# Kernel optimization log

Hardware: AMD Instinct MI355X
Metric: run time of the kernel (lower is better)

## Reference

```python
import jax, jax.numpy as jnp
import numpy as np
import math

D_MODEL = 256; N_LEVELS = 5; N_HEADS = 8; N_POINTS = 4
D_HEAD = D_MODEL // N_HEADS
BS = 1; T = 5; H = 64; W = 96


def conv3x3(x, w, b):
    # x: (N, C, H, W), w: (O, C, 3, 3) -> SAME padding conv
    y = jax.lax.conv_general_dilated(x, w, (1, 1), ((1, 1), (1, 1)),
                                     dimension_numbers=('NCHW', 'OIHW', 'NCHW'))
    return y + b[None, :, None, None]


def bilinear_zero(img, px, py):
    # img: (C, Hh, Ww); px, py: (...) pixel coords; zero padding outside.
    C, Hh, Ww = img.shape
    x0 = jnp.floor(px); y0 = jnp.floor(py)
    wx1 = px - x0; wx0 = 1.0 - wx1
    wy1 = py - y0; wy0 = 1.0 - wy1

    def gather(xi, yi):
        valid = (xi >= 0) & (xi < Ww) & (yi >= 0) & (yi < Hh)
        xc = jnp.clip(xi, 0, Ww - 1).astype(jnp.int32)
        yc = jnp.clip(yi, 0, Hh - 1).astype(jnp.int32)
        return img[:, yc, xc] * valid.astype(img.dtype)

    return (gather(x0, y0) * (wx0 * wy0) + gather(x0 + 1, y0) * (wx1 * wy0)
            + gather(x0, y0 + 1) * (wx0 * wy1) + gather(x0 + 1, y0 + 1) * (wx1 * wy1))


def warp(x, flo):
    # x: (b, c, h, w), flo: (b, 2, h, w); grid_sample(align_corners=True) equivalent
    b, c, h, w = x.shape
    gy, gx = jnp.meshgrid(jnp.arange(h, dtype=x.dtype), jnp.arange(w, dtype=x.dtype), indexing='ij')
    px = gx[None] + flo[:, 0]
    py = gy[None] + flo[:, 1]
    return jax.vmap(bilinear_zero)(x, px, py)


def flow_guid_offset(ff, fb, offset):
    # ff, fb: (b, 4, 2, h, w); offset: (N, T*h*w, heads, L, P, 2)
    N, THW, heads, L, P, _ = offset.shape
    hw = THW // L
    off = offset.reshape(N, L, hw, heads, L, P, 2)
    f01, f12, f23, f34 = ff[:, 0], ff[:, 1], ff[:, 2], ff[:, 3]
    f02 = f01 + warp(f12, f01)
    f03 = f02 + warp(f23, f02)
    f04 = f03 + warp(f34, f03)
    f13 = f12 + warp(f23, f12)
    f14 = f13 + warp(f34, f13)
    f24 = f23 + warp(f34, f23)
    b10, b21, b32, b43 = fb[:, 0], fb[:, 1], fb[:, 2], fb[:, 3]
    b42 = b43 + warp(b32, b43)
    b41 = b42 + warp(b21, b42)
    b40 = b41 + warp(b10, b41)
    b31 = b32 + warp(b21, b32)
    b30 = b31 + warp(b10, b31)
    b20 = b21 + warp(b10, b21)

    def flat(f):  # (b, 2, h, w) -> (b, hw, 2)
        return f.transpose(0, 2, 3, 1).reshape(f.shape[0], -1, 2)

    z = jnp.zeros_like(flat(f01))
    adds = jnp.stack([
        jnp.stack([z, flat(f01), flat(f02), flat(f03), flat(f04)], axis=2),
        jnp.stack([flat(b10), z, flat(f12), flat(f13), flat(f14)], axis=2),
        jnp.stack([flat(b20), flat(b21), z, flat(f23), flat(f24)], axis=2),
        jnp.stack([flat(b30), flat(b31), flat(b32), z, flat(f34)], axis=2),
        # NOTE: source repeats chunk3's flows for chunk4 (kept faithfully)
        jnp.stack([flat(b30), flat(b31), flat(b32), z, flat(f34)], axis=2),
    ], axis=1)  # (b, L, hw, L, 2)
    off = off + adds[:, :, :, None, :, None, :]
    return off.reshape(N, THW, heads, L, P, 2)


def _forward(query, input_flatten, reference_points, input_spatial_shapes,
             input_level_start_index, input_padding_mask, flow_forward, flow_backward,
             w_off, b_off, w_attn, b_attn, w_val, b_val, w_out, b_out):
    bs, t, c, h, w = query.shape
    q2 = query.reshape(bs * t, c, h, w)
    value = conv3x3(input_flatten.reshape(bs * t, c, h, w), w_val, b_val)
    off = conv3x3(q2, w_off, b_off)      # (bs*t, heads*L*P*2, h, w)
    aw = conv3x3(q2, w_attn, b_attn)     # (bs*t, heads*L*P, h, w)
    Lq = t * h * w

    def to_tokens(x):  # (bs*t, C, h, w) -> (bs, t*h*w, C)
        return x.reshape(bs, t, -1, h * w).transpose(0, 1, 3, 2).reshape(bs, Lq, -1)

    value = to_tokens(value)
    off = to_tokens(off)
    aw = to_tokens(aw)
    value = jnp.where(input_padding_mask[..., None], jnp.zeros((), value.dtype), value)
    value = value.reshape(bs, Lq, N_HEADS, D_HEAD)
    off = off.reshape(bs, Lq, N_HEADS, N_LEVELS, N_POINTS, 2)
    off = flow_guid_offset(flow_forward, flow_backward, off)
    aw = jax.nn.softmax(aw.reshape(bs, Lq, N_HEADS, N_LEVELS * N_POINTS), axis=-1)
    aw = aw.reshape(bs, Lq, N_HEADS, N_LEVELS, N_POINTS)
    # sampling locations, normalized by (W_l, H_l)
    normalizer = jnp.stack([input_spatial_shapes[:, 1], input_spatial_shapes[:, 0]], -1).astype(off.dtype)
    loc = reference_points[:, :, None, :, None, :] + off / normalizer[None, None, None, :, None, :]
    # core: multi-scale deformable bilinear sampling (grid_sample align_corners=False)
    value_lvl = value.reshape(bs, t, h * w, N_HEADS, D_HEAD)
    out = jnp.zeros((bs * N_HEADS, D_HEAD, Lq), dtype=value.dtype)
    for lvl in range(N_LEVELS):
        v = value_lvl[:, lvl].reshape(bs, h, w, N_HEADS, D_HEAD)
        v = v.transpose(0, 3, 4, 1, 2).reshape(bs * N_HEADS, D_HEAD, h, w)
        l = loc[:, :, :, lvl]  # (bs, Lq, heads, P, 2)
        px = (l[..., 0] * w - 0.5).transpose(0, 2, 1, 3).reshape(bs * N_HEADS, Lq, N_POINTS)
        py = (l[..., 1] * h - 0.5).transpose(0, 2, 1, 3).reshape(bs * N_HEADS, Lq, N_POINTS)
        samp = jax.vmap(bilinear_zero)(v, px, py)  # (bs*heads, D_HEAD, Lq, P)
        w_l = aw[:, :, :, lvl].transpose(0, 2, 1, 3).reshape(bs * N_HEADS, 1, Lq, N_POINTS)
        out = out + jnp.sum(samp * w_l, axis=-1)
    out = out.reshape(bs, N_HEADS, D_HEAD, Lq).transpose(0, 3, 1, 2).reshape(bs, Lq, c)
    out = out.reshape(bs, t, h * w, c).transpose(0, 1, 3, 2).reshape(bs * t, c, h, w)
    out = conv3x3(out, w_out, b_out)
    return out.reshape(bs, t, c, h, w)


def setup_inputs() -> dict:
    key = jax.random.key(0)
    ks = jax.random.split(key, 10)
    Lq = T * H * W
    query = jax.random.normal(ks[0], (BS, T, D_MODEL, H, W), jnp.float32)
    input_flatten = jax.random.normal(ks[1], (BS, T, D_MODEL, H, W), jnp.float32)
    reference_points = jax.random.uniform(ks[2], (BS, Lq, N_LEVELS, 2), jnp.float32)
    input_spatial_shapes = jnp.tile(jnp.array([[H, W]], jnp.int32), (N_LEVELS, 1))
    input_level_start_index = jnp.arange(N_LEVELS, dtype=jnp.int32) * (H * W)
    input_padding_mask = jnp.zeros((BS, Lq), dtype=bool)
    flow_forward = jax.random.normal(ks[3], (BS, 4, 2, H, W), jnp.float32) * 2.0
    flow_backward = jax.random.normal(ks[4], (BS, 4, 2, H, W), jnp.float32) * 2.0

    def xavier(k, shape):
        fan_in = shape[1] * shape[2] * shape[3]
        fan_out = shape[0] * shape[2] * shape[3]
        lim = math.sqrt(6.0 / (fan_in + fan_out))
        return jax.random.uniform(k, shape, jnp.float32, -lim, lim)

    w_off = jax.random.normal(ks[5], (N_HEADS * N_LEVELS * N_POINTS * 2, D_MODEL, 3, 3), jnp.float32) * 0.01
    # bias init follows _reset_parameters grid_init
    thetas = np.arange(N_HEADS) * (2.0 * np.pi / N_HEADS)
    grid = np.stack([np.cos(thetas), np.sin(thetas)], -1)
    grid = grid / np.abs(grid).max(-1, keepdims=True)
    grid = np.tile(grid.reshape(N_HEADS, 1, 1, 2), (1, N_LEVELS, N_POINTS, 1))
    for i in range(N_POINTS):
        grid[:, :, i, :] *= i + 1
    b_off = jnp.asarray(grid.reshape(-1), jnp.float32)
    w_attn = jax.random.normal(ks[6], (N_HEADS * N_LEVELS * N_POINTS, D_MODEL, 3, 3), jnp.float32) * 0.01
    b_attn = jnp.zeros((N_HEADS * N_LEVELS * N_POINTS,), jnp.float32)
    w_val = xavier(ks[7], (D_MODEL, D_MODEL, 3, 3)); b_val = jnp.zeros((D_MODEL,), jnp.float32)
    w_out = xavier(ks[8], (D_MODEL, D_MODEL, 3, 3)); b_out = jnp.zeros((D_MODEL,), jnp.float32)
    return {"query": query, "input_flatten": input_flatten, "reference_points": reference_points,
            "input_spatial_shapes": input_spatial_shapes, "input_level_start_index": input_level_start_index,
            "input_padding_mask": input_padding_mask, "flow_forward": flow_forward, "flow_backward": flow_backward,
            "w_off": w_off, "b_off": b_off, "w_attn": w_attn, "b_attn": b_attn,
            "w_val": w_val, "b_val": b_val, "w_out": w_out, "b_out": b_out}


def reference(query, input_flatten, reference_points, input_spatial_shapes,
              input_level_start_index, input_padding_mask, flow_forward, flow_backward,
              w_off, b_off, w_attn, b_attn, w_val, b_val, w_out, b_out):
    return _forward(query, input_flatten, reference_points, input_spatial_shapes,
                    input_level_start_index, input_padding_mask, flow_forward, flow_backward,
                    w_off, b_off, w_attn, b_attn, w_val, b_val, w_out, b_out)
```

## Files before the change

### kernel.cpp

```cpp
#include <hip/hip_runtime.h>
#include <hip/hip_bf16.h>
#include <hip/hip_fp16.h>

typedef __hip_bfloat16 bf16;
typedef __attribute__((ext_vector_type(8))) short short8;
typedef __attribute__((ext_vector_type(4))) float float4v;

#define T_  5
#define H_  64
#define W_  96
#define HW_ (H_*W_)
#define C_  256
#define NH_ 8
#define DH_ 32
#define NL_ 5
#define NP_ 4
#define LQ_ (T_*HW_)
#define UNITS_ (LQ_*NH_)

#define PH_ 66
#define PW_ 98

static __device__ __forceinline__ void gl2lds16(const bf16* g, bf16* l){
  __builtin_amdgcn_global_load_lds(
      (const __attribute__((address_space(1))) unsigned int*)g,
      (__attribute__((address_space(3))) unsigned int*)l, 16, 0, 0);
}

__global__ __launch_bounds__(256) void zfill_k(float4* __restrict__ p, int n4){
  int i = blockIdx.x*256 + threadIdx.x;
  if (i < n4){ float4 z; z.x=z.y=z.z=z.w=0.f; p[i]=z; }
}

__global__ __launch_bounds__(256) void pad_in_k(const float* __restrict__ in0,
                                                const float* __restrict__ in1,
                                                bf16* __restrict__ pad0,
                                                bf16* __restrict__ pad1){
  __shared__ bf16 sb[256][66];
  const float* in = blockIdx.z ? in1 : in0;
  bf16* pad       = blockIdx.z ? pad1 : pad0;
  int t = blockIdx.y;
  int pix0 = blockIdx.x*64;
  int tid = threadIdx.x;
  int pl = tid & 63, cg = tid >> 6;
  #pragma unroll 4
  for (int it=0; it<64; ++it){
    int c = it*4 + cg;
    sb[c][pl] = __float2bfloat16(in[((size_t)t*C_ + c)*HW_ + pix0 + pl]);
  }
  __syncthreads();
  for (int p=0; p<64; ++p){
    int pix = pix0 + p;
    int y = pix/W_, x = pix - y*W_;
    pad[(((size_t)t*PH_ + y+1)*PW_ + x+1)*C_ + tid] = sb[tid][p];
  }
}

#define S0_ 589824
#define S1_ 1179648
__global__ __launch_bounds__(256) void wt_all_k(const float* __restrict__ wv,
                                                const float* __restrict__ wo,
                                                const float* __restrict__ wa,
                                                const float* __restrict__ wout,
                                                const float* __restrict__ bo,
                                                const float* __restrict__ ba,
                                                bf16* __restrict__ WTv,
                                                bf16* __restrict__ WToa,
                                                bf16* __restrict__ WTout,
                                                float* __restrict__ boa){
  int idx = blockIdx.x*256 + threadIdx.x;
  if (idx < S0_){
    int n = idx/2304, r = idx - n*2304; int tap = r>>8, ci = r&255;
    WTv[idx] = __float2bfloat16(wv[((size_t)(n*C_+ci))*9 + tap]);
  } else if (idx < S0_+S1_){
    int k = idx - S0_;
    int n = k/2304, r = k - n*2304; int tap=r>>8, ci=r&255;
    float v = 0.f;
    if (n < 320)      v = wo[((size_t)(n*C_+ci))*9+tap];
    else if (n < 480) v = wa[((size_t)((n-320)*C_+ci))*9+tap];
    WToa[k] = __float2bfloat16(v);
  } else if (idx < S0_+S1_+S0_){
    int k = idx - S0_ - S1_;
    int n = k/2304, r = k - n*2304; int tap=r>>8, ci=r&255;
    WTout[k] = __float2bfloat16(wout[((size_t)(n*C_+ci))*9+tap]);
  } else if (idx < S0_+S1_+S0_+512){
    int n = idx - (S0_+S1_+S0_);
    float v = 0.f;
    if (n < 320) v = bo[n]; else if (n < 480) v = ba[n-320];
    boa[n] = v;
  }
}

#define BM 128
#define BN 256
#define BK 64

__global__ __launch_bounds__(256,2) void gemm12_k(const bf16* __restrict__ Av,
                                                  const bf16* __restrict__ Aq,
                                                  const bf16* __restrict__ WTv,
                                                  const bf16* __restrict__ WToa,
                                                  const float* __restrict__ bv,
                                                  const float* __restrict__ boa,
                                                  bf16* __restrict__ outv,
                                                  float* __restrict__ P,
                                                  float* __restrict__ aw){
  __shared__ __align__(16) bf16 As[BM*BK];
  __shared__ __align__(16) bf16 Bs[BN*BK];
  int tid = threadIdx.x;
  int lane = tid & 63, wvi = tid >> 6;
  int wm = wvi & 1, wn = wvi >> 1;
  int quad = lane >> 4, l15 = lane & 15;
  int bx = blockIdx.x, byy = blockIdx.y;
  bool isval = byy == 0;
  const bf16* Apad  = isval ? Av  : Aq;
  const bf16* WT    = isval ? WTv : WToa;
  const float* bias = isval ? bv  : boa;
  int nby = isval ? 0 : byy - 1;

  int srow = tid >> 3;
  int c8   = (tid & 7) ^ (srow & 7);
  long abase[4];
  #pragma unroll
  for (int j=0;j<4;++j){
    int p = j*32 + srow;
    int Pm = bx*BM + p;
    int t = Pm / HW_, rem = Pm - t*HW_;
    int y = rem / W_, x = rem - y*W_;
    abase[j] = ((long)(t*PH_ + y)*PW_ + x)*C_ + c8*8;
  }
  const bf16* bbase = WT + (size_t)(nby*BN + srow)*2304 + c8*8;

  float4v acc[4][8];
  #pragma unroll
  for (int jn=0;jn<8;++jn){
    float bvv = bias[nby*BN + wn*128 + jn*16 + l15];
    #pragma unroll
    for (int i=0;i<4;++i){ acc[i][jn][0]=bvv; acc[i][jn][1]=bvv; acc[i][jn][2]=bvv; acc[i][jn][3]=bvv; }
  }

  for (int kt=0; kt<36; ++kt){
    int tap = kt >> 2, kc = (kt & 3) << 6;
    int dy = tap/3, dx = tap - dy*3;
    long ash = (long)(dy*PW_ + dx)*C_ + kc;
    long bsh = (long)kt*64;
    __syncthreads();
    #pragma unroll
    for (int j=0;j<4;++j)
      gl2lds16(Apad + abase[j] + ash, As + (j*256+tid)*8);
    #pragma unroll
    for (int j=0;j<8;++j)
      gl2lds16(bbase + (size_t)j*32*2304 + bsh, Bs + (j*256+tid)*8);
    __syncthreads();
    #pragma unroll
    for (int kk=0; kk<2; ++kk){
      int slot = ((kk<<2) + quad) ^ (l15 & 7);
      short8 af[4], bfr[8];
      #pragma unroll
      for (int jn=0;jn<8;++jn)
        bfr[jn] = *(const short8*)(Bs + (wn*128 + jn*16 + l15)*BK + slot*8);
      #pragma unroll
      for (int i=0;i<4;++i)
        af[i] = *(const short8*)(As + (wm*64 + i*16 + l15)*BK + slot*8);
      #pragma unroll
      for (int i=0;i<4;++i)
        #pragma unroll
        for (int jn=0;jn<8;++jn)
          acc[i][jn] = __builtin_amdgcn_mfma_f32_16x16x32_bf16(af[i], bfr[jn], acc[i][jn], 0,0,0);
    }
  }

  #pragma unroll
  for (int i=0;i<4;++i){
    int mr = bx*BM + wm*64 + i*16 + quad*4;
    #pragma unroll
    for (int jn=0;jn<8;++jn){
      int nc = nby*BN + wn*128 + jn*16 + l15;
      #pragma unroll
      for (int r=0;r<4;++r){
        float v = acc[i][jn][r];
        long m = mr + r;
        if (isval){
          outv[m*256 + nc] = __float2bfloat16(v);
        } else {
          if (nc < 320){
            int h = nc/40, rr = nc - h*40;
            int l = rr >> 3, pxy = rr & 7;
            P[((size_t)l*UNITS_ + m*8 + h)*8 + pxy] = v;
          } else if (nc < 480){
            int hh = (nc-320)/20, ii = (nc-320) - hh*20;
            aw[((size_t)m*8 + hh)*20 + ii] = v;
          }
        }
      }
    }
  }
}

__global__ __launch_bounds__(256,2) void gemm_out_k(const bf16* __restrict__ Apad,
                                                    const bf16* __restrict__ WT,
                                                    const float* __restrict__ bias,
                                                    float* __restrict__ out){
  __shared__ __align__(16) bf16 As[BM*BK];
  __shared__ __align__(16) bf16 Bs[BN*BK];
  int tid = threadIdx.x;
  int lane = tid & 63, wvi = tid >> 6;
  int wm = wvi & 1, wn = wvi >> 1;
  int quad = lane >> 4, l15 = lane & 15;
  int bx = blockIdx.x;

  int srow = tid >> 3;
  int c8   = (tid & 7) ^ (srow & 7);
  long abase[4];
  #pragma unroll
  for (int j=0;j<4;++j){
    int p = j*32 + srow;
    int Pm = bx*BM + p;
    int t = Pm / HW_, rem = Pm - t*HW_;
    int y = rem / W_, x = rem - y*W_;
    abase[j] = ((long)(t*PH_ + y)*PW_ + x)*C_ + c8*8;
  }
  const bf16* bbase = WT + (size_t)srow*2304 + c8*8;

  float4v acc[4][8];
  #pragma unroll
  for (int jn=0;jn<8;++jn){
    float bvv = bias[wn*128 + jn*16 + l15];
    #pragma unroll
    for (int i=0;i<4;++i){ acc[i][jn][0]=bvv; acc[i][jn][1]=bvv; acc[i][jn][2]=bvv; acc[i][jn][3]=bvv; }
  }

  for (int kt=0; kt<36; ++kt){
    int tap = kt >> 2, kc = (kt & 3) << 6;
    int dy = tap/3, dx = tap - dy*3;
    long ash = (long)(dy*PW_ + dx)*C_ + kc;
    long bsh = (long)kt*64;
    __syncthreads();
    #pragma unroll
    for (int j=0;j<4;++j)
      gl2lds16(Apad + abase[j] + ash, As + (j*256+tid)*8);
    #pragma unroll
    for (int j=0;j<8;++j)
      gl2lds16(bbase + (size_t)j*32*2304 + bsh, Bs + (j*256+tid)*8);
    __syncthreads();
    #pragma unroll
    for (int kk=0; kk<2; ++kk){
      int slot = ((kk<<2) + quad) ^ (l15 & 7);
      short8 af[4], bfr[8];
      #pragma unroll
      for (int jn=0;jn<8;++jn)
        bfr[jn] = *(const short8*)(Bs + (wn*128 + jn*16 + l15)*BK + slot*8);
      #pragma unroll
      for (int i=0;i<4;++i)
        af[i] = *(const short8*)(As + (wm*64 + i*16 + l15)*BK + slot*8);
      #pragma unroll
      for (int i=0;i<4;++i)
        #pragma unroll
        for (int jn=0;jn<8;++jn)
          acc[i][jn] = __builtin_amdgcn_mfma_f32_16x16x32_bf16(af[i], bfr[jn], acc[i][jn], 0,0,0);
    }
  }

  int t = (bx*BM) / HW_;
  #pragma unroll
  for (int i=0;i<4;++i){
    int m = bx*BM + wm*64 + i*16 + quad*4;
    int pix = m - t*HW_;
    #pragma unroll
    for (int jn=0;jn<8;++jn){
      int nc = wn*128 + jn*16 + l15;
      *(float4v*)(out + ((size_t)(t*C_ + nc))*HW_ + pix) = acc[i][jn];
    }
  }
}

static __device__ __forceinline__ float bilin2(const float* __restrict__ img,
                                               float px, float py){
  float x0f = floorf(px), y0f = floorf(py);
  int x0 = (int)x0f, y0 = (int)y0f;
  float fx = px - x0f, fy = py - y0f;
  int x1 = x0+1, y1 = y0+1;
  bool vx0 = (x0>=0)&&(x0<W_), vx1 = (x1>=0)&&(x1<W_);
  bool vy0 = (y0>=0)&&(y0<H_), vy1 = (y1>=0)&&(y1<H_);
  float c00 = (vx0&&vy0)? img[y0*W_+x0] : 0.f;
  float c10 = (vx1&&vy0)? img[y0*W_+x1] : 0.f;
  float c01 = (vx0&&vy1)? img[y1*W_+x0] : 0.f;
  float c11 = (vx1&&vy1)? img[y1*W_+x1] : 0.f;
  return c00*(1.f-fx)*(1.f-fy) + c10*fx*(1.f-fy) + c01*(1.f-fx)*fy + c11*fx*fy;
}

__global__ __launch_bounds__(256) void flow_init_k(const float* __restrict__ ff,
                                                   const float* __restrict__ fb,
                                                   float* __restrict__ flows){
  int i = blockIdx.x*256 + threadIdx.x;
  const int per = 2*HW_;
  if (i >= 7*per) return;
  int f = i/per, r = i - f*per;
  float v; int slot;
  if (f < 4) { v = ff[f*per + r]; slot = f; }
  else       { v = fb[(f-4)*per + r]; slot = 10+(f-4); }
  flows[slot*per + r] = v;
}

struct Comps { int dst[5]; int a[5]; int src[5]; };

__global__ __launch_bounds__(256) void flow_compose_k(float* __restrict__ flows, Comps c){
  int ci  = blockIdx.y;
  int pix = blockIdx.x*256 + threadIdx.x;
  float* D       = flows + c.dst[ci]*2*HW_;
  const float* A = flows + c.a[ci]  *2*HW_;
  const float* S = flows + c.src[ci]*2*HW_;
  float ax = A[pix], ay = A[HW_+pix];
  float px = (float)(pix % W_) + ax;
  float py = (float)(pix / W_) + ay;
  D[pix]      = ax + bilin2(S,      px, py);
  D[HW_+pix]  = ay + bilin2(S+HW_,  px, py);
}

__device__ const int g_slotTab[25] = {
  -1,  0,  4,  5,  6,
  10, -1,  1,  7,  8,
  13, 11, -1,  2,  9,
  15, 14, 12, -1,  3,
  15, 14, 12, -1,  3 };

__global__ __launch_bounds__(256) void prep_k(const float* __restrict__ aw,
                                              const float* __restrict__ ref,
                                              const float* __restrict__ flows,
                                              float* __restrict__ P,
                                              __half* __restrict__ w16){
  int unit = blockIdx.x*256 + threadIdx.x;
  const float4* p4 = (const float4*)(aw + (size_t)unit*20);
  float4 v[5];
  #pragma unroll
  for (int i=0;i<5;++i) v[i] = p4[i];
  float* e = (float*)v;
  float m = -1e30f;
  #pragma unroll
  for (int i=0;i<20;++i) m = fmaxf(m, e[i]);
  float s = 0.f;
  #pragma unroll
  for (int i=0;i<20;++i){ e[i] = __expf(e[i]-m); s += e[i]; }
  float inv = 1.f/s;
  __half2* o2 = (__half2*)(w16 + (size_t)unit*20);
  #pragma unroll
  for (int i=0;i<10;++i)
    o2[i] = __floats2half2_rn(e[2*i]*inv, e[2*i+1]*inv);

  int q = unit >> 3;
  int t_q = q / HW_, pix = q - t_q*HW_;
  #pragma unroll
  for (int l=0; l<NL_; ++l){
    int slot = g_slotTab[t_q*5+l];
    float ax=0.f, ay=0.f;
    if (slot >= 0){ ax = flows[slot*2*HW_ + pix]; ay = flows[slot*2*HW_ + HW_ + pix]; }
    float bx = ref[(q*5+l)*2+0]*(float)W_ - 0.5f + ax;
    float by = ref[(q*5+l)*2+1]*(float)H_ - 0.5f + ay;
    float2* pp = (float2*)(P + ((size_t)l*UNITS_ + unit)*8);
    #pragma unroll
    for (int p=0;p<4;++p){ float2 t = pp[p]; t.x += bx; t.y += by; pp[p] = t; }
  }
}

template<bool FIRST, bool LAST>
__global__ __launch_bounds__(256) void phase_k(const unsigned* __restrict__ vimg0,
                                               const float2*  __restrict__ Pl,
                                               const __half*  __restrict__ wl,
                                               __half2* __restrict__ acc,
                                               bf16* __restrict__ attn_pad){
  __shared__ float4 sW[16][4];
  __shared__ int4   sI[16][4];
  int tid = threadIdx.x;
  if (tid < 64){
    int g = tid >> 2, p = tid & 3;
    int unit = blockIdx.x*16 + g;
    float2 pp = Pl[(size_t)unit*4 + p];
    float w = __half2float(wl[(size_t)unit*20 + p]);
    float x0f = floorf(pp.x), y0f = floorf(pp.y);
    float fx = pp.x - x0f,    fy = pp.y - y0f;
    int x0 = (int)x0f, y0 = (int)y0f;
    int x1 = x0+1, y1 = y0+1;
    float wx0 = 1.f-fx, wx1 = fx, wy0 = 1.f-fy, wy1 = fy;
    if ((unsigned)x0 >= (unsigned)W_) wx0 = 0.f;
    if ((unsigned)x1 >= (unsigned)W_) wx1 = 0.f;
    if ((unsigned)y0 >= (unsigned)H_) wy0 = 0.f;
    if ((unsigned)y1 >= (unsigned)H_) wy1 = 0.f;
    int xc0 = min(max(x0,0),W_-1), xc1 = min(max(x1,0),W_-1);
    int yc0 = min(max(y0,0),H_-1), yc1 = min(max(y1,0),H_-1);
    sW[g][p] = make_float4(w*wx0*wy0, w*wx1*wy0, w*wx0*wy1, w*wx1*wy1);
    sI[g][p] = make_int4((yc0*W_+xc0)*128, (yc0*W_+xc1)*128,
                         (yc1*W_+xc0)*128, (yc1*W_+xc1)*128);
  }
  __syncthreads();
  int g = tid >> 4, e = tid & 15;
  int unit = blockIdx.x*16 + g;
  int q = unit >> 3, h = unit & 7;
  const unsigned* vimg = vimg0 + h*16 + e;
  float a0, a1;
  if (FIRST){ a0 = 0.f; a1 = 0.f; }
  else { __half2 c = acc[(size_t)unit*16 + e]; a0 = __low2float(c); a1 = __high2float(c); }
  #pragma unroll
  for (int p=0; p<4; ++p){
    float4 w4 = sW[g][p];
    int4   i4 = sI[g][p];
    unsigned u00 = vimg[i4.x], u10 = vimg[i4.y];
    unsigned u01 = vimg[i4.z], u11 = vimg[i4.w];
    union {unsigned v; float f;} lo, hi;
    lo.v = u00<<16; hi.v = u00 & 0xffff0000u;
    a0 = fmaf(w4.x, lo.f, a0); a1 = fmaf(w4.x, hi.f, a1);
    lo.v = u10<<16; hi.v = u10 & 0xffff0000u;
    a0 = fmaf(w4.y, lo.f, a0); a1 = fmaf(w4.y, hi.f, a1);
    lo.v = u01<<16; hi.v = u01 & 0xffff0000u;
    a0 = fmaf(w4.z, lo.f, a0); a1 = fmaf(w4.z, hi.f, a1);
    lo.v = u11<<16; hi.v = u11 & 0xffff0000u;
    a0 = fmaf(w4.w, lo.f, a0); a1 = fmaf(w4.w, hi.f, a1);
  }
  if (LAST){
    int t_q = q / HW_, pix = q - t_q*HW_;
    int yq = pix / W_, xq = pix - yq*W_;
    union {unsigned u; bf16 hh[2];} pk;
    pk.hh[0] = __float2bfloat16(a0);
    pk.hh[1] = __float2bfloat16(a1);
    *(unsigned*)(attn_pad + (((size_t)t_q*PH_ + yq+1)*PW_ + xq+1)*C_ + h*DH_ + e*2) = pk.u;
  } else {
    acc[(size_t)unit*16 + e] = __floats2half2_rn(a0, a1);
  }
}

extern "C" void kernel_launch(void* const* d_in, const int* in_sizes, int n_in,
                              void* d_out, int out_size, void* d_ws, size_t ws_size,
                              hipStream_t stream) {
  const float* query   = (const float*)d_in[0];
  const float* in_flat = (const float*)d_in[1];
  const float* refpts  = (const float*)d_in[2];
  const float* ff      = (const float*)d_in[6];
  const float* fb      = (const float*)d_in[7];
  const float* w_off   = (const float*)d_in[8];
  const float* b_off   = (const float*)d_in[9];
  const float* w_attn  = (const float*)d_in[10];
  const float* b_attn  = (const float*)d_in[11];
  const float* w_val   = (const float*)d_in[12];
  const float* b_val   = (const float*)d_in[13];
  const float* w_out   = (const float*)d_in[14];
  const float* b_out   = (const float*)d_in[15];
  float* out = (float*)d_out;

  char* ws = (char*)d_ws;
  bf16*  v_pad   = (bf16*) (ws + 0);
  bf16*  q_pad   = (bf16*) (ws + 16558080);
  __half* w16    = (__half*)(ws + 16558080);
  bf16*  v_val   = (bf16*) (ws + 33116160);
  float* P       = (float*)(ws + 48844800);
  float* v_aw    = (float*)(ws + 88166400);
  __half2* acc   = (__half2*)(ws + 88166400);
  float* v_flows = (float*)(ws + 107827200);
  bf16*  WT_val  = (bf16*) (ws + 108613632);
  bf16*  WT_oa   = (bf16*) (ws + 109793280);
  bf16*  WT_out  = (bf16*) (ws + 112152576);
  float* bias_oa = (float*)(ws + 113332224);
  bf16*  attn_pad = v_pad;
  if (ws_size < (size_t)113334272) return;

  zfill_k<<<(2069760+255)/256, 256, 0, stream>>>((float4*)v_pad, 2069760);

  wt_all_k<<<(S0_+S1_+S0_+512+255)/256, 256, 0, stream>>>(
      w_val, w_off, w_attn, w_out, b_off, b_attn, WT_val, WT_oa, WT_out, bias_oa);

  flow_init_k<<<(7*2*HW_+255)/256, 256, 0, stream>>>(ff, fb, v_flows);
  Comps A;
  A.dst[0]=4;  A.a[0]=0;  A.src[0]=1;
  A.dst[1]=7;  A.a[1]=1;  A.src[1]=2;
  A.dst[2]=9;  A.a[2]=2;  A.src[2]=3;
  A.dst[3]=13; A.a[3]=11; A.src[3]=10;
  A.dst[4]=14; A.a[4]=12; A.src[4]=11;
  flow_compose_k<<<dim3(HW_/256,5), 256, 0, stream>>>(v_flows, A);
  Comps B;
  B.dst[0]=5;  B.a[0]=4;  B.src[0]=2;
  B.dst[1]=8;  B.a[1]=7;  B.src[1]=3;
  B.dst[2]=15; B.a[2]=14; B.src[2]=10;
  B.dst[3]=0;  B.a[3]=0;  B.src[3]=0;
  B.dst[4]=0;  B.a[4]=0;  B.src[4]=0;
  flow_compose_k<<<dim3(HW_/256,3), 256, 0, stream>>>(v_flows, B);
  Comps Cc;
  Cc.dst[0]=6; Cc.a[0]=5; Cc.src[0]=3;
  Cc.dst[1]=0; Cc.a[1]=0; Cc.src[1]=0;
  Cc.dst[2]=0; Cc.a[2]=0; Cc.src[2]=0;
  Cc.dst[3]=0; Cc.a[3]=0; Cc.src[3]=0;
  Cc.dst[4]=0; Cc.a[4]=0; Cc.src[4]=0;
  flow_compose_k<<<dim3(HW_/256,1), 256, 0, stream>>>(v_flows, Cc);

  pad_in_k<<<dim3(HW_/64, T_, 2), 256, 0, stream>>>(in_flat, query, v_pad, q_pad);

  gemm12_k<<<dim3(240, 3), 256, 0, stream>>>(v_pad, q_pad, WT_val, WT_oa,
                                             b_val, bias_oa, v_val, P, v_aw);

  prep_k<<<UNITS_/256, 256, 0, stream>>>(v_aw, refpts, v_flows, P, w16);

  {
    const unsigned* vb = (const unsigned*)v_val;
    phase_k<true ,false><<<UNITS_/16, 256, 0, stream>>>(vb + 0ul*HW_*128,
        (const float2*)(P + 0ul*UNITS_*8), w16 + 0,  acc, attn_pad);
    phase_k<false,false><<<UNITS_/16, 256, 0, stream>>>(vb + 1ul*HW_*128,
        (const float2*)(P + 1ul*UNITS_*8), w16 + 4,  acc, attn_pad);
    phase_k<false,false><<<UNITS_/16, 256, 0, stream>>>(vb + 2ul*HW_*128,
        (const float2*)(P + 2ul*UNITS_*8), w16 + 8,  acc, attn_pad);
    phase_k<false,false><<<UNITS_/16, 256, 0, stream>>>(vb + 3ul*HW_*128,
        (const float2*)(P + 3ul*UNITS_*8), w16 + 12, acc, attn_pad);
    phase_k<false,true ><<<UNITS_/16, 256, 0, stream>>>(vb + 4ul*HW_*128,
        (const float2*)(P + 4ul*UNITS_*8), w16 + 16, acc, attn_pad);
  }

  gemm_out_k<<<dim3(240, 1), 256, 0, stream>>>(attn_pad, WT_out, b_out, out);
}
```

Baseline: 484.9 us.

## Fuse setup kernels into one megakernel and move offset base into phase kernels

Result: faster. 451.9 us (-6.8%).

```diff
diff --git a/kernel.cpp b/kernel.cpp
--- a/kernel.cpp
+++ b/kernel.cpp
@@ -27,67 +27,178 @@
       (__attribute__((address_space(3))) unsigned int*)l, 16, 0, 0);
 }
 
-__global__ __launch_bounds__(256) void zfill_k(float4* __restrict__ p, int n4){
-  int i = blockIdx.x*256 + threadIdx.x;
-  if (i < n4){ float4 z; z.x=z.y=z.z=z.w=0.f; p[i]=z; }
-}
-
-__global__ __launch_bounds__(256) void pad_in_k(const float* __restrict__ in0,
-                                                const float* __restrict__ in1,
-                                                bf16* __restrict__ pad0,
-                                                bf16* __restrict__ pad1){
-  __shared__ bf16 sb[256][66];
-  const float* in = blockIdx.z ? in1 : in0;
-  bf16* pad       = blockIdx.z ? pad1 : pad0;
-  int t = blockIdx.y;
-  int pix0 = blockIdx.x*64;
-  int tid = threadIdx.x;
-  int pl = tid & 63, cg = tid >> 6;
-  #pragma unroll 4
-  for (int it=0; it<64; ++it){
-    int c = it*4 + cg;
-    sb[c][pl] = __float2bfloat16(in[((size_t)t*C_ + c)*HW_ + pix0 + pl]);
-  }
-  __syncthreads();
-  for (int p=0; p<64; ++p){
-    int pix = pix0 + p;
-    int y = pix/W_, x = pix - y*W_;
-    pad[(((size_t)t*PH_ + y+1)*PW_ + x+1)*C_ + tid] = sb[tid][p];
-  }
-}
-
-#define S0_ 589824
-#define S1_ 1179648
-__global__ __launch_bounds__(256) void wt_all_k(const float* __restrict__ wv,
-                                                const float* __restrict__ wo,
-                                                const float* __restrict__ wa,
-                                                const float* __restrict__ wout,
-                                                const float* __restrict__ bo,
-                                                const float* __restrict__ ba,
-                                                bf16* __restrict__ WTv,
-                                                bf16* __restrict__ WToa,
-                                                bf16* __restrict__ WTout,
-                                                float* __restrict__ boa){
-  int idx = blockIdx.x*256 + threadIdx.x;
-  if (idx < S0_){
-    int n = idx/2304, r = idx - n*2304; int tap = r>>8, ci = r&255;
-    WTv[idx] = __float2bfloat16(wv[((size_t)(n*C_+ci))*9 + tap]);
-  } else if (idx < S0_+S1_){
-    int k = idx - S0_;
-    int n = k/2304, r = k - n*2304; int tap=r>>8, ci=r&255;
-    float v = 0.f;
-    if (n < 320)      v = wo[((size_t)(n*C_+ci))*9+tap];
-    else if (n < 480) v = wa[((size_t)((n-320)*C_+ci))*9+tap];
-    WToa[k] = __float2bfloat16(v);
-  } else if (idx < S0_+S1_+S0_){
-    int k = idx - S0_ - S1_;
-    int n = k/2304, r = k - n*2304; int tap=r>>8, ci=r&255;
-    WTout[k] = __float2bfloat16(wout[((size_t)(n*C_+ci))*9+tap]);
-  } else if (idx < S0_+S1_+S0_+512){
-    int n = idx - (S0_+S1_+S0_);
-    float v = 0.f;
-    if (n < 320) v = bo[n]; else if (n < 480) v = ba[n-320];
-    boa[n] = v;
+static __device__ __forceinline__ float bilin2(const float* __restrict__ img,
+                                               float px, float py){
+  float x0f = floorf(px), y0f = floorf(py);
+  int x0 = (int)x0f, y0 = (int)y0f;
+  float fx = px - x0f, fy = py - y0f;
+  int x1 = x0+1, y1 = y0+1;
+  bool vx0 = (x0>=0)&&(x0<W_), vx1 = (x1>=0)&&(x1<W_);
+  bool vy0 = (y0>=0)&&(y0<H_), vy1 = (y1>=0)&&(y1<H_);
+  float c00 = (vx0&&vy0)? img[y0*W_+x0] : 0.f;
+  float c10 = (vx1&&vy0)? img[y0*W_+x1] : 0.f;
+  float c01 = (vx0&&vy1)? img[y1*W_+x0] : 0.f;
+  float c11 = (vx1&&vy1)? img[y1*W_+x1] : 0.f;
+  return c00*(1.f-fx)*(1.f-fy) + c10*fx*(1.f-fy) + c01*(1.f-fx)*fy + c11*fx*fy;
+}
+
+#define MG_PAD   960
+#define MG_WT    1025
+#define MG_INIT  336
+#define MG_FA    120
+#define MG_BZ    405
+__global__ __launch_bounds__(256) void mega0_k(
+    const float* __restrict__ in0, const float* __restrict__ in1,
+    bf16* __restrict__ pad0, bf16* __restrict__ pad1,
+    const float* __restrict__ wv, const float* __restrict__ wo,
+    const float* __restrict__ wa, const float* __restrict__ wout,
+    const float* __restrict__ bo, const float* __restrict__ ba,
+    bf16* __restrict__ WTv, bf16* __restrict__ WToa, bf16* __restrict__ WTout,
+    float* __restrict__ boa,
+    const float* __restrict__ ff, const float* __restrict__ fb,
+    float* __restrict__ flows)
+{
+  __shared__ __align__(16) char smem[33792];
+  int b = blockIdx.x, tid = threadIdx.x;
+  if (b < MG_PAD){
+    bf16 (*sb)[66] = (bf16(*)[66])smem;
+    int z = b / 480, r = b - z*480;
+    int t = r / 96, bxp = r - t*96;
+    const float* in = z ? in1 : in0;
+    bf16* pad       = z ? pad1 : pad0;
+    int pix0 = bxp*64;
+    int pl = tid & 63, cg = tid >> 6;
+    #pragma unroll 4
+    for (int it=0; it<64; ++it){
+      int c = it*4 + cg;
+      sb[c][pl] = __float2bfloat16(in[((size_t)t*C_ + c)*HW_ + pix0 + pl]);
+    }
+    __syncthreads();
+    for (int p=0; p<64; ++p){
+      int pix = pix0 + p;
+      int y = pix/W_, x = pix - y*W_;
+      pad[(((size_t)t*PH_ + y+1)*PW_ + x+1)*C_ + tid] = sb[tid][p];
+    }
+    return;
+  }
+  b -= MG_PAD;
+  if (b < MG_WT){
+    if (b == 1024){
+      #pragma unroll
+      for (int k=0;k<2;++k){
+        int n = tid + k*256;
+        float v = 0.f;
+        if (n < 320) v = bo[n]; else if (n < 480) v = ba[n-320];
+        boa[n] = v;
+      }
+      return;
+    }
+    float* ld = (float*)smem;
+    const float* src; bf16* dst;
+    if (b < 256){ src = wv + (size_t)b*2304; dst = WTv + (size_t)b*2304; }
+    else if (b < 768){
+      int n = b-256; dst = WToa + (size_t)n*2304;
+      src = (n<320) ? (wo + (size_t)n*2304)
+          : ((n<480) ? (wa + (size_t)(n-320)*2304) : (const float*)0);
+    } else { int n = b-768; src = wout + (size_t)n*2304; dst = WTout + (size_t)n*2304; }
+    if (src){
+      #pragma unroll
+      for (int k=0;k<9;++k) ld[tid + k*256] = src[tid + k*256];
+      __syncthreads();
+      #pragma unroll
+      for (int k=0;k<9;++k){
+        int o = tid + k*256; int tap = o >> 8, ci = o & 255;
+        dst[o] = __float2bfloat16(ld[ci*9 + tap]);
+      }
+    } else {
+      #pragma unroll
+      for (int k=0;k<9;++k) dst[tid + k*256] = __float2bfloat16(0.f);
+    }
+    return;
+  }
+  b -= MG_WT;
+  if (b < MG_INIT){
+    int i = b*256 + tid;
+    const int per = 2*HW_;
+    int f = i/per, r = i - f*per;
+    if (f < 4) flows[f*per + r]          = ff[i];
+    else       flows[(10+(f-4))*per + r] = fb[(f-4)*per + r];
+    return;
+  }
+  b -= MG_INIT;
+  if (b < MG_FA){
+    int ci = b / 24;
+    int pix = (b - ci*24)*256 + tid;
+    const int dsts[5] = {4,7,9,13,14};
+    const float* A; const float* S;
+    switch(ci){
+      case 0: A = ff;          S = ff + 2*HW_; break;
+      case 1: A = ff + 2*HW_;  S = ff + 4*HW_; break;
+      case 2: A = ff + 4*HW_;  S = ff + 6*HW_; break;
+      case 3: A = fb + 2*HW_;  S = fb;         break;
+      default:A = fb + 4*HW_;  S = fb + 2*HW_; break;
+    }
+    float* D = flows + dsts[ci]*2*HW_;
+    float ax = A[pix], ay = A[HW_+pix];
+    float px = (float)(pix % W_) + ax;
+    float py = (float)(pix / W_) + ay;
+    D[pix]      = ax + bilin2(S,      px, py);
+    D[HW_+pix]  = ay + bilin2(S+HW_,  px, py);
+    return;
+  }
+  b -= MG_FA;
+  {
+    int idx = b*256 + tid;
+    int pair = idx / 10368, r = idx - pair*10368;
+    int pxi = r >> 5, q8 = r & 31;
+    int t = pair >> 1, z = pair & 1;
+    int y, x;
+    if (pxi < 98){ y = 0;  x = pxi; }
+    else if (pxi < 196){ y = 65; x = pxi-98; }
+    else if (pxi < 260){ y = pxi-196+1; x = 0; }
+    else { y = pxi-260+1; x = 97; }
+    bf16* pad = z ? pad1 : pad0;
+    uint4 zz; zz.x = zz.y = zz.z = zz.w = 0u;
+    *(uint4*)(pad + (((size_t)t*PH_ + y)*PW_ + x)*C_ + q8*8) = zz;
+  }
+}
+
+__global__ __launch_bounds__(256) void flowBC_k(const float* __restrict__ ff,
+                                                const float* __restrict__ fb,
+                                                float* __restrict__ flows){
+  int gy = blockIdx.y;
+  int pix = blockIdx.x*256 + threadIdx.x;
+  float gx = (float)(pix % W_), gyy = (float)(pix / W_);
+  if (gy == 0){
+    const float* A   = flows + 4*2*HW_;
+    const float* S23 = ff + 4*HW_;
+    const float* S34 = ff + 6*HW_;
+    float ax = A[pix], ay = A[HW_+pix];
+    float px = gx + ax, py = gyy + ay;
+    float c3x = ax + bilin2(S23,      px, py);
+    float c3y = ay + bilin2(S23+HW_,  px, py);
+    float* D3 = flows + 5*2*HW_;
+    D3[pix] = c3x; D3[HW_+pix] = c3y;
+    px = gx + c3x; py = gyy + c3y;
+    float* D4 = flows + 6*2*HW_;
+    D4[pix]     = c3x + bilin2(S34,     px, py);
+    D4[HW_+pix] = c3y + bilin2(S34+HW_, px, py);
+  } else if (gy == 1){
+    const float* A = flows + 7*2*HW_;
+    const float* S = ff + 6*HW_;
+    float ax = A[pix], ay = A[HW_+pix];
+    float px = gx + ax, py = gyy + ay;
+    float* D = flows + 8*2*HW_;
+    D[pix]     = ax + bilin2(S,     px, py);
+    D[HW_+pix] = ay + bilin2(S+HW_, px, py);
+  } else {
+    const float* A = flows + 14*2*HW_;
+    const float* S = fb;
+    float ax = A[pix], ay = A[HW_+pix];
+    float px = gx + ax, py = gyy + ay;
+    float* D = flows + 15*2*HW_;
+    D[pix]     = ax + bilin2(S,     px, py);
+    D[HW_+pix] = ay + bilin2(S+HW_, px, py);
   }
 }
 
@@ -273,49 +384,6 @@
   }
 }
 
-static __device__ __forceinline__ float bilin2(const float* __restrict__ img,
-                                               float px, float py){
-  float x0f = floorf(px), y0f = floorf(py);
-  int x0 = (int)x0f, y0 = (int)y0f;
-  float fx = px - x0f, fy = py - y0f;
-  int x1 = x0+1, y1 = y0+1;
-  bool vx0 = (x0>=0)&&(x0<W_), vx1 = (x1>=0)&&(x1<W_);
-  bool vy0 = (y0>=0)&&(y0<H_), vy1 = (y1>=0)&&(y1<H_);
-  float c00 = (vx0&&vy0)? img[y0*W_+x0] : 0.f;
-  float c10 = (vx1&&vy0)? img[y0*W_+x1] : 0.f;
-  float c01 = (vx0&&vy1)? img[y1*W_+x0] : 0.f;
-  float c11 = (vx1&&vy1)? img[y1*W_+x1] : 0.f;
-  return c00*(1.f-fx)*(1.f-fy) + c10*fx*(1.f-fy) + c01*(1.f-fx)*fy + c11*fx*fy;
-}
-
-__global__ __launch_bounds__(256) void flow_init_k(const float* __restrict__ ff,
-                                                   const float* __restrict__ fb,
-                                                   float* __restrict__ flows){
-  int i = blockIdx.x*256 + threadIdx.x;
-  const int per = 2*HW_;
-  if (i >= 7*per) return;
-  int f = i/per, r = i - f*per;
-  float v; int slot;
-  if (f < 4) { v = ff[f*per + r]; slot = f; }
-  else       { v = fb[(f-4)*per + r]; slot = 10+(f-4); }
-  flows[slot*per + r] = v;
-}
-
-struct Comps { int dst[5]; int a[5]; int src[5]; };
-
-__global__ __launch_bounds__(256) void flow_compose_k(float* __restrict__ flows, Comps c){
-  int ci  = blockIdx.y;
-  int pix = blockIdx.x*256 + threadIdx.x;
-  float* D       = flows + c.dst[ci]*2*HW_;
-  const float* A = flows + c.a[ci]  *2*HW_;
-  const float* S = flows + c.src[ci]*2*HW_;
-  float ax = A[pix], ay = A[HW_+pix];
-  float px = (float)(pix % W_) + ax;
-  float py = (float)(pix / W_) + ay;
-  D[pix]      = ax + bilin2(S,      px, py);
-  D[HW_+pix]  = ay + bilin2(S+HW_,  px, py);
-}
-
 __device__ const int g_slotTab[25] = {
   -1,  0,  4,  5,  6,
   10, -1,  1,  7,  8,
@@ -324,9 +392,6 @@
   15, 14, 12, -1,  3 };
 
 __global__ __launch_bounds__(256) void prep_k(const float* __restrict__ aw,
-                                              const float* __restrict__ ref,
-                                              const float* __restrict__ flows,
-                                              float* __restrict__ P,
                                               __half* __restrict__ w16){
   int unit = blockIdx.x*256 + threadIdx.x;
   const float4* p4 = (const float4*)(aw + (size_t)unit*20);
@@ -345,26 +410,15 @@
   #pragma unroll
   for (int i=0;i<10;++i)
     o2[i] = __floats2half2_rn(e[2*i]*inv, e[2*i+1]*inv);
-
-  int q = unit >> 3;
-  int t_q = q / HW_, pix = q - t_q*HW_;
-  #pragma unroll
-  for (int l=0; l<NL_; ++l){
-    int slot = g_slotTab[t_q*5+l];
-    float ax=0.f, ay=0.f;
-    if (slot >= 0){ ax = flows[slot*2*HW_ + pix]; ay = flows[slot*2*HW_ + HW_ + pix]; }
-    float bx = ref[(q*5+l)*2+0]*(float)W_ - 0.5f + ax;
-    float by = ref[(q*5+l)*2+1]*(float)H_ - 0.5f + ay;
-    float2* pp = (float2*)(P + ((size_t)l*UNITS_ + unit)*8);
-    #pragma unroll
-    for (int p=0;p<4;++p){ float2 t = pp[p]; t.x += bx; t.y += by; pp[p] = t; }
-  }
 }
 
 template<bool FIRST, bool LAST>
 __global__ __launch_bounds__(256) void phase_k(const unsigned* __restrict__ vimg0,
                                                const float2*  __restrict__ Pl,
                                                const __half*  __restrict__ wl,
+                                               const float*   __restrict__ ref,
+                                               const float*   __restrict__ flows,
+                                               int lvl,
                                                __half2* __restrict__ acc,
                                                bf16* __restrict__ attn_pad){
   __shared__ float4 sW[16][4];
@@ -373,10 +427,17 @@
   if (tid < 64){
     int g = tid >> 2, p = tid & 3;
     int unit = blockIdx.x*16 + g;
-    float2 pp = Pl[(size_t)unit*4 + p];
+    float2 pr = Pl[(size_t)unit*4 + p];
     float w = __half2float(wl[(size_t)unit*20 + p]);
-    float x0f = floorf(pp.x), y0f = floorf(pp.y);
-    float fx = pp.x - x0f,    fy = pp.y - y0f;
+    int q = unit >> 3;
+    int t_q = q / HW_, pix = q - t_q*HW_;
+    int slot = g_slotTab[t_q*5 + lvl];
+    float ax = 0.f, ay = 0.f;
+    if (slot >= 0){ ax = flows[slot*2*HW_ + pix]; ay = flows[slot*2*HW_ + HW_ + pix]; }
+    float ppx = pr.x + ref[(q*5+lvl)*2+0]*(float)W_ - 0.5f + ax;
+    float ppy = pr.y + ref[(q*5+lvl)*2+1]*(float)H_ - 0.5f + ay;
+    float x0f = floorf(ppx), y0f = floorf(ppy);
+    float fx = ppx - x0f,    fy = ppy - y0f;
     int x0 = (int)x0f, y0 = (int)y0f;
     int x1 = x0+1, y1 = y0+1;
     float wx0 = 1.f-fx, wx1 = fx, wy0 = 1.f-fy, wy1 = fy;
@@ -460,53 +521,30 @@
   bf16*  attn_pad = v_pad;
   if (ws_size < (size_t)113334272) return;
 
-  zfill_k<<<(2069760+255)/256, 256, 0, stream>>>((float4*)v_pad, 2069760);
-
-  wt_all_k<<<(S0_+S1_+S0_+512+255)/256, 256, 0, stream>>>(
-      w_val, w_off, w_attn, w_out, b_off, b_attn, WT_val, WT_oa, WT_out, bias_oa);
-
-  flow_init_k<<<(7*2*HW_+255)/256, 256, 0, stream>>>(ff, fb, v_flows);
-  Comps A;
-  A.dst[0]=4;  A.a[0]=0;  A.src[0]=1;
-  A.dst[1]=7;  A.a[1]=1;  A.src[1]=2;
-  A.dst[2]=9;  A.a[2]=2;  A.src[2]=3;
-  A.dst[3]=13; A.a[3]=11; A.src[3]=10;
-  A.dst[4]=14; A.a[4]=12; A.src[4]=11;
-  flow_compose_k<<<dim3(HW_/256,5), 256, 0, stream>>>(v_flows, A);
-  Comps B;
-  B.dst[0]=5;  B.a[0]=4;  B.src[0]=2;
-  B.dst[1]=8;  B.a[1]=7;  B.src[1]=3;
-  B.dst[2]=15; B.a[2]=14; B.src[2]=10;
-  B.dst[3]=0;  B.a[3]=0;  B.src[3]=0;
-  B.dst[4]=0;  B.a[4]=0;  B.src[4]=0;
-  flow_compose_k<<<dim3(HW_/256,3), 256, 0, stream>>>(v_flows, B);
-  Comps Cc;
-  Cc.dst[0]=6; Cc.a[0]=5; Cc.src[0]=3;
-  Cc.dst[1]=0; Cc.a[1]=0; Cc.src[1]=0;
-  Cc.dst[2]=0; Cc.a[2]=0; Cc.src[2]=0;
-  Cc.dst[3]=0; Cc.a[3]=0; Cc.src[3]=0;
-  Cc.dst[4]=0; Cc.a[4]=0; Cc.src[4]=0;
-  flow_compose_k<<<dim3(HW_/256,1), 256, 0, stream>>>(v_flows, Cc);
-
-  pad_in_k<<<dim3(HW_/64, T_, 2), 256, 0, stream>>>(in_flat, query, v_pad, q_pad);
+  mega0_k<<<MG_PAD+MG_WT+MG_INIT+MG_FA+MG_BZ, 256, 0, stream>>>(
+      in_flat, query, v_pad, q_pad,
+      w_val, w_off, w_attn, w_out, b_off, b_attn,
+      WT_val, WT_oa, WT_out, bias_oa, ff, fb, v_flows);
+
+  flowBC_k<<<dim3(HW_/256, 3), 256, 0, stream>>>(ff, fb, v_flows);
 
   gemm12_k<<<dim3(240, 3), 256, 0, stream>>>(v_pad, q_pad, WT_val, WT_oa,
                                              b_val, bias_oa, v_val, P, v_aw);
 
-  prep_k<<<UNITS_/256, 256, 0, stream>>>(v_aw, refpts, v_flows, P, w16);
+  prep_k<<<UNITS_/256, 256, 0, stream>>>(v_aw, w16);
 
   {
     const unsigned* vb = (const unsigned*)v_val;
     phase_k<true ,false><<<UNITS_/16, 256, 0, stream>>>(vb + 0ul*HW_*128,
-        (const float2*)(P + 0ul*UNITS_*8), w16 + 0,  acc, attn_pad);
+        (const float2*)(P + 0ul*UNITS_*8), w16 + 0,  refpts, v_flows, 0, acc, attn_pad);
     phase_k<false,false><<<UNITS_/16, 256, 0, stream>>>(vb + 1ul*HW_*128,
-        (const float2*)(P + 1ul*UNITS_*8), w16 + 4,  acc, attn_pad);
+        (const float2*)(P + 1ul*UNITS_*8), w16 + 4,  refpts, v_flows, 1, acc, attn_pad);
     phase_k<false,false><<<UNITS_/16, 256, 0, stream>>>(vb + 2ul*HW_*128,
-        (const float2*)(P + 2ul*UNITS_*8), w16 + 8,  acc, attn_pad);
+        (const float2*)(P + 2ul*UNITS_*8), w16 + 8,  refpts, v_flows, 2, acc, attn_pad);
     phase_k<false,false><<<UNITS_/16, 256, 0, stream>>>(vb + 3ul*HW_*128,
-        (const float2*)(P + 3ul*UNITS_*8), w16 + 12, acc, attn_pad);
+        (const float2*)(P + 3ul*UNITS_*8), w16 + 12, refpts, v_flows, 3, acc, attn_pad);
     phase_k<false,true ><<<UNITS_/16, 256, 0, stream>>>(vb + 4ul*HW_*128,
-        (const float2*)(P + 4ul*UNITS_*8), w16 + 16, acc, attn_pad);
+        (const float2*)(P + 4ul*UNITS_*8), w16 + 16, refpts, v_flows, 4, acc, attn_pad);
   }
 
   gemm_out_k<<<dim3(240, 1), 256, 0, stream>>>(attn_pad, WT_out, b_out, out);
```
